# Kernel tuning notes

Measured on AMD Instinct MI355X. Metric: run time of the kernel, lower is better.

The kernel has to match this reference:

```python
import jax, jax.numpy as jnp
import numpy as np

B, S, DIN, DOUT, A, T, H = 8, 1024, 1024, 1024, 4, 4, 8  # arity A, T cell types, hidden H


def setup_inputs() -> dict:
    key = jax.random.key(0)
    ks = jax.random.split(key, 6)
    x = jax.random.normal(ks[0], (B, S, DIN), jnp.float32)
    sc = 1.0 / np.sqrt(DIN).astype(np.float32)
    weight = jax.random.uniform(ks[1], (A * DOUT, DIN), jnp.float32, -sc, sc)
    bias = jax.random.uniform(ks[2], (A * DOUT,), jnp.float32, -sc, sc)
    # stacked per-cell-type MLP params: arity -> H -> 1 (tanh)
    cw1 = jax.random.normal(ks[3], (T, A, H), jnp.float32) / np.sqrt(A).astype(np.float32)
    cb1 = jnp.zeros((T, H), jnp.float32)
    cw2 = jax.random.normal(ks[4], (T, H), jnp.float32) / np.sqrt(H).astype(np.float32)
    cb2 = jnp.zeros((T,), jnp.float32)
    return {"x": x, "weight": weight, "bias": bias,
            "cw1": cw1, "cb1": cb1, "cw2": cw2, "cb2": cb2}


def reference(x, weight, bias, cw1, cb1, cw2, cb2):
    T_, A_, H_ = cw1.shape
    Dout = weight.shape[0] // A_
    G = Dout // T_  # neurons per cell type (cell_indices = contiguous blocks via np.repeat)
    # all_inputs = F.linear(input, weight, bias): (B, S, A*Dout)
    z = jnp.einsum('bsd,od->bso', x, weight) + bias
    # slice per-neuron arity chunks -> (B, S, T, G, A)
    z = z.reshape(z.shape[0], z.shape[1], T_, G, A_)
    # per-cell-type MLP applied to every neuron of that type (replaces Python loop)
    h = jnp.tanh(jnp.einsum('bstga,tah->bstgh', z, cw1) + cb1[:, None, :])
    o = jnp.einsum('bstgh,th->bstg', h, cw2) + cb2[:, None]
    # concat over neurons -> (B, S, Dout)
    return o.reshape(o.shape[0], o.shape[1], Dout)
```

## Files before the change

### kernel.cpp

```cpp
#include <hip/hip_runtime.h>


typedef __bf16 bf16x8 __attribute__((ext_vector_type(8)));
typedef float f32x4 __attribute__((ext_vector_type(4)));

#define BM 128
#define BN 128
#define BK 64
#define KDIM 1024
#define ZSTRIDE 132
#define XN8 (8192 * 1024 / 8)
#define WN8 (4096 * 1024 / 8)

__global__ __launch_bounds__(256) void cvt_bf16_kernel(
    const float* __restrict__ x, const float* __restrict__ w,
    __bf16* __restrict__ xb, __bf16* __restrict__ wb) {
    int i = blockIdx.x * 256 + threadIdx.x;
    const float* src;
    __bf16* dst;
    int j;
    if (i < XN8) { src = x; dst = xb; j = i; }
    else         { src = w; dst = wb; j = i - XN8; }
    const f32x4* p = (const f32x4*)src + 2 * (size_t)j;
    f32x4 a = p[0], b = p[1];
    bf16x8 o;
    o[0] = (__bf16)a[0]; o[1] = (__bf16)a[1]; o[2] = (__bf16)a[2]; o[3] = (__bf16)a[3];
    o[4] = (__bf16)b[0]; o[5] = (__bf16)b[1]; o[6] = (__bf16)b[2]; o[7] = (__bf16)b[3];
    ((bf16x8*)dst)[j] = o;
}

union __align__(16) SmemU {
    __bf16 stg[BM * BK + BN * BK];
    float  z[64 * ZSTRIDE];
};

__global__ __launch_bounds__(256) void fused_gemm_mlp_kernel(
    const __bf16* __restrict__ Ag,
    const __bf16* __restrict__ Bg,
    const float* __restrict__ bias,
    const float* __restrict__ cw1,
    const float* __restrict__ cb1,
    const float* __restrict__ cw2,
    const float* __restrict__ cb2,
    float* __restrict__ out)
{
    __shared__ SmemU u;

    const int tid  = threadIdx.x;
    const int wave = tid >> 6;
    const int lane = tid & 63;
    const int wm = wave >> 1;
    const int wn = wave & 1;
    const int bn0 = blockIdx.x * BN;
    const int bm0 = blockIdx.y * BM;

    f32x4 acc[4][4] = {};

    const int srow = lane >> 3;
    const int scol8 = (((lane & 7) ^ srow) * 8);

    const int lr = lane & 15;
    const int lk = lane >> 4;
    const int lx = lane & 7;
    int aoff[2][4], boff[2][4];
#pragma unroll
    for (int kh = 0; kh < 2; ++kh)
#pragma unroll
        for (int mi = 0; mi < 4; ++mi) {
            const int cidx = kh * 4 + lk;
            aoff[kh][mi] = (wm * 64 + mi * 16 + lr) * BK + ((cidx ^ lx) * 8);
            boff[kh][mi] = BM * BK + (wn * 64 + mi * 16 + lr) * BK + ((cidx ^ lx) * 8);
        }

    for (int k0 = 0; k0 < KDIM; k0 += BK) {
#pragma unroll
        for (int c = 0; c < 4; ++c) {
            const int chunk = wave + c * 4;
            const __bf16* ga = Ag + (size_t)(bm0 + chunk * 8 + srow) * KDIM + k0 + scol8;
            __builtin_amdgcn_global_load_lds(
                (__attribute__((address_space(1))) void*)ga,
                (__attribute__((address_space(3))) void*)&u.stg[chunk * 8 * BK],
                16, 0, 0);
            const __bf16* gb = Bg + (size_t)(bn0 + chunk * 8 + srow) * KDIM + k0 + scol8;
            __builtin_amdgcn_global_load_lds(
                (__attribute__((address_space(1))) void*)gb,
                (__attribute__((address_space(3))) void*)&u.stg[BM * BK + chunk * 8 * BK],
                16, 0, 0);
        }
        __syncthreads();

#pragma unroll
        for (int kh = 0; kh < 2; ++kh) {
            bf16x8 af[4], bfr[4];
#pragma unroll
            for (int mi = 0; mi < 4; ++mi) af[mi] = *(const bf16x8*)&u.stg[aoff[kh][mi]];
#pragma unroll
            for (int ni = 0; ni < 4; ++ni) bfr[ni] = *(const bf16x8*)&u.stg[boff[kh][ni]];
#pragma unroll
            for (int mi = 0; mi < 4; ++mi)
#pragma unroll
                for (int ni = 0; ni < 4; ++ni)
                    acc[mi][ni] = __builtin_amdgcn_mfma_f32_16x16x32_bf16(
                        af[mi], bfr[ni], acc[mi][ni], 0, 0, 0);
        }
        __syncthreads();
    }

    const int t = bn0 >> 10;
    float w1[32], b1[8], w2[8];
#pragma unroll
    for (int i = 0; i < 32; ++i) w1[i] = cw1[t * 32 + i];
#pragma unroll
    for (int i = 0; i < 8; ++i) { b1[i] = cb1[t * 8 + i]; w2[i] = cw2[t * 8 + i]; }
    const float b2 = cb2[t];

    float bcol[4];
#pragma unroll
    for (int ni = 0; ni < 4; ++ni)
        bcol[ni] = bias[bn0 + wn * 64 + ni * 16 + lr];

    const float L2E2 = 2.885390081777927f;

#pragma unroll
    for (int h = 0; h < 2; ++h) {
        if (wm == h) {
#pragma unroll
            for (int ni = 0; ni < 4; ++ni) {
                const int n = wn * 64 + ni * 16 + lr;
#pragma unroll
                for (int mi = 0; mi < 4; ++mi) {
                    const int r = mi * 16 + lk * 4;
                    f32x4 v = acc[mi][ni];
                    u.z[(r + 0) * ZSTRIDE + n] = v[0] + bcol[ni];
                    u.z[(r + 1) * ZSTRIDE + n] = v[1] + bcol[ni];
                    u.z[(r + 2) * ZSTRIDE + n] = v[2] + bcol[ni];
                    u.z[(r + 3) * ZSTRIDE + n] = v[3] + bcol[ni];
                }
            }
        }
        __syncthreads();

#pragma unroll
        for (int it = 0; it < 8; ++it) {
            const int i = tid + it * 256;
            const int q = i & 31;
            const int r = i >> 5;
            f32x4 z = *(const f32x4*)&u.z[r * ZSTRIDE + 4 * q];
            float o = 0.f;
#pragma unroll
            for (int hh = 0; hh < 8; ++hh) {
                float pre = z[0] * w1[0 * 8 + hh] + z[1] * w1[1 * 8 + hh]
                          + z[2] * w1[2 * 8 + hh] + z[3] * w1[3 * 8 + hh] + b1[hh];
                float e = __builtin_amdgcn_exp2f(pre * L2E2);
                float th = 1.0f - 2.0f * __builtin_amdgcn_rcpf(e + 1.0f);
                o += th * w2[hh];
            }
            o += b2;
            out[(size_t)(bm0 + h * 64 + r) * 1024 + (bn0 >> 2) + q] = o;
        }
        __syncthreads();
    }
}

extern "C" void kernel_launch(void* const* d_in, const int* in_sizes, int n_in,
                              void* d_out, int out_size, void* d_ws, size_t ws_size,
                              hipStream_t stream) {
    const float* x    = (const float*)d_in[0];
    const float* w    = (const float*)d_in[1];
    const float* bias = (const float*)d_in[2];
    const float* cw1  = (const float*)d_in[3];
    const float* cb1  = (const float*)d_in[4];
    const float* cw2  = (const float*)d_in[5];
    const float* cb2  = (const float*)d_in[6];
    float* out = (float*)d_out;

    __bf16* xb = (__bf16*)d_ws;
    __bf16* wb = xb + (size_t)8192 * 1024;

    cvt_bf16_kernel<<<(XN8 + WN8) / 256, 256, 0, stream>>>(x, w, xb, wb);

    dim3 grid(4096 / BN, 8192 / BM);
    fused_gemm_mlp_kernel<<<grid, 256, 0, stream>>>(xb, wb, bias, cw1, cb1, cw2, cb2, out);
}
```

Baseline: 204.0 us.

## Use 256x128 block tile with 32x32x16 MFMA and wider per-wave tiles

```diff
diff --git a/kernel.cpp b/kernel.cpp
--- a/kernel.cpp
+++ b/kernel.cpp
@@ -3,11 +3,13 @@
 
 typedef __bf16 bf16x8 __attribute__((ext_vector_type(8)));
 typedef float f32x4 __attribute__((ext_vector_type(4)));
+typedef float f32x16 __attribute__((ext_vector_type(16)));
 
-#define BM 128
+#define BM 256
 #define BN 128
 #define BK 64
 #define KDIM 1024
+#define A_ELEMS (BM * BK)
 #define ZSTRIDE 132
 #define XN8 (8192 * 1024 / 8)
 #define WN8 (4096 * 1024 / 8)
@@ -30,11 +32,11 @@
 }
 
 union __align__(16) SmemU {
-    __bf16 stg[BM * BK + BN * BK];
+    __bf16 stg[A_ELEMS + BN * BK];
     float  z[64 * ZSTRIDE];
 };
 
-__global__ __launch_bounds__(256) void fused_gemm_mlp_kernel(
+__global__ __launch_bounds__(256, 2) void fused_gemm_mlp_kernel(
     const __bf16* __restrict__ Ag,
     const __bf16* __restrict__ Bg,
     const float* __restrict__ bias,
@@ -54,53 +56,58 @@
     const int bn0 = blockIdx.x * BN;
     const int bm0 = blockIdx.y * BM;
 
-    f32x4 acc[4][4] = {};
+    f32x16 acc[4][2] = {};
 
-    const int srow = lane >> 3;
+    const int srow  = lane >> 3;
     const int scol8 = (((lane & 7) ^ srow) * 8);
 
-    const int lr = lane & 15;
-    const int lk = lane >> 4;
-    const int lx = lane & 7;
-    int aoff[2][4], boff[2][4];
+    const int lr5 = lane & 31;
+    const int lk2 = lane >> 5;
+    const int lx  = lane & 7;
+    int a_base[4], b_base[4];
 #pragma unroll
-    for (int kh = 0; kh < 2; ++kh)
-#pragma unroll
-        for (int mi = 0; mi < 4; ++mi) {
-            const int cidx = kh * 4 + lk;
-            aoff[kh][mi] = (wm * 64 + mi * 16 + lr) * BK + ((cidx ^ lx) * 8);
-            boff[kh][mi] = BM * BK + (wn * 64 + mi * 16 + lr) * BK + ((cidx ^ lx) * 8);
-        }
+    for (int kh = 0; kh < 4; ++kh) {
+        const int cx = ((kh * 2 + lk2) ^ lx) * 16;
+        a_base[kh] = (wm * 128 + lr5) * (BK * 2) + cx;
+        b_base[kh] = A_ELEMS * 2 + (wn * 64 + lr5) * (BK * 2) + cx;
+    }
+    const char* sb = (const char*)u.stg;
 
     for (int k0 = 0; k0 < KDIM; k0 += BK) {
 #pragma unroll
-        for (int c = 0; c < 4; ++c) {
+        for (int c = 0; c < 8; ++c) {
             const int chunk = wave + c * 4;
             const __bf16* ga = Ag + (size_t)(bm0 + chunk * 8 + srow) * KDIM + k0 + scol8;
             __builtin_amdgcn_global_load_lds(
                 (__attribute__((address_space(1))) void*)ga,
                 (__attribute__((address_space(3))) void*)&u.stg[chunk * 8 * BK],
                 16, 0, 0);
+        }
+#pragma unroll
+        for (int c = 0; c < 4; ++c) {
+            const int chunk = wave + c * 4;
             const __bf16* gb = Bg + (size_t)(bn0 + chunk * 8 + srow) * KDIM + k0 + scol8;
             __builtin_amdgcn_global_load_lds(
                 (__attribute__((address_space(1))) void*)gb,
-                (__attribute__((address_space(3))) void*)&u.stg[BM * BK + chunk * 8 * BK],
+                (__attribute__((address_space(3))) void*)&u.stg[A_ELEMS + chunk * 8 * BK],
                 16, 0, 0);
         }
         __syncthreads();
 
 #pragma unroll
-        for (int kh = 0; kh < 2; ++kh) {
-            bf16x8 af[4], bfr[4];
+        for (int kh = 0; kh < 4; ++kh) {
+            bf16x8 af[4], bfr[2];
 #pragma unroll
-            for (int mi = 0; mi < 4; ++mi) af[mi] = *(const bf16x8*)&u.stg[aoff[kh][mi]];
+            for (int mi = 0; mi < 4; ++mi)
+                af[mi] = *(const bf16x8*)(sb + a_base[kh] + mi * 4096);
 #pragma unroll
-            for (int ni = 0; ni < 4; ++ni) bfr[ni] = *(const bf16x8*)&u.stg[boff[kh][ni]];
+            for (int ni = 0; ni < 2; ++ni)
+                bfr[ni] = *(const bf16x8*)(sb + b_base[kh] + ni * 4096);
 #pragma unroll
             for (int mi = 0; mi < 4; ++mi)
 #pragma unroll
-                for (int ni = 0; ni < 4; ++ni)
-                    acc[mi][ni] = __builtin_amdgcn_mfma_f32_16x16x32_bf16(
+                for (int ni = 0; ni < 2; ++ni)
+                    acc[mi][ni] = __builtin_amdgcn_mfma_f32_32x32x16_bf16(
                         af[mi], bfr[ni], acc[mi][ni], 0, 0, 0);
         }
         __syncthreads();
@@ -114,27 +121,31 @@
     for (int i = 0; i < 8; ++i) { b1[i] = cb1[t * 8 + i]; w2[i] = cw2[t * 8 + i]; }
     const float b2 = cb2[t];
 
-    float bcol[4];
+    float bcol[2];
 #pragma unroll
-    for (int ni = 0; ni < 4; ++ni)
-        bcol[ni] = bias[bn0 + wn * 64 + ni * 16 + lr];
+    for (int ni = 0; ni < 2; ++ni)
+        bcol[ni] = bias[bn0 + wn * 64 + ni * 32 + lr5];
 
     const float L2E2 = 2.885390081777927f;
 
 #pragma unroll
-    for (int h = 0; h < 2; ++h) {
-        if (wm == h) {
+    for (int h = 0; h < 4; ++h) {
+        if (wm == (h >> 1)) {
+            const int mi0 = (h & 1) * 2;
 #pragma unroll
-            for (int ni = 0; ni < 4; ++ni) {
-                const int n = wn * 64 + ni * 16 + lr;
+            for (int dmi = 0; dmi < 2; ++dmi) {
+                const int mi = mi0 + dmi;
 #pragma unroll
-                for (int mi = 0; mi < 4; ++mi) {
-                    const int r = mi * 16 + lk * 4;
-                    f32x4 v = acc[mi][ni];
-                    u.z[(r + 0) * ZSTRIDE + n] = v[0] + bcol[ni];
-                    u.z[(r + 1) * ZSTRIDE + n] = v[1] + bcol[ni];
-                    u.z[(r + 2) * ZSTRIDE + n] = v[2] + bcol[ni];
-                    u.z[(r + 3) * ZSTRIDE + n] = v[3] + bcol[ni];
+                for (int ni = 0; ni < 2; ++ni) {
+                    const int n = wn * 64 + ni * 32 + lr5;
+#pragma unroll
+                    for (int g = 0; g < 4; ++g) {
+                        const int rb = dmi * 32 + g * 8 + lk2 * 4;
+                        u.z[(rb + 0) * ZSTRIDE + n] = acc[mi][ni][g * 4 + 0] + bcol[ni];
+                        u.z[(rb + 1) * ZSTRIDE + n] = acc[mi][ni][g * 4 + 1] + bcol[ni];
+                        u.z[(rb + 2) * ZSTRIDE + n] = acc[mi][ni][g * 4 + 2] + bcol[ni];
+                        u.z[(rb + 3) * ZSTRIDE + n] = acc[mi][ni][g * 4 + 3] + bcol[ni];
+                    }
                 }
             }
         }
```

Measured after the change: 188.1 us. 7.8% less time.
